# Performance work log

Measured on AMD Instinct MI355X. Metric: run time of the kernel, lower is better.

## Reference

```python
import jax, jax.numpy as jnp
import numpy as np

N_NODES = 100000


def gcn_conv(x, W, b, src, dst, n_nodes):
    """PyG GCNConv: out = D^{-1/2} (A + I) D^{-1/2} X W + b."""
    h = x @ W  # [N, F_out]
    # add self-loops
    loop = jnp.arange(n_nodes, dtype=src.dtype)
    s = jnp.concatenate([src, loop])
    d = jnp.concatenate([dst, loop])
    # symmetric normalization (deg counts incoming edges incl. self-loop)
    deg = jax.ops.segment_sum(jnp.ones_like(d, dtype=h.dtype), d, num_segments=n_nodes)
    dinv = jnp.where(deg > 0, jax.lax.rsqrt(deg), 0.0)
    coef = dinv[s] * dinv[d]  # [E+N]
    msg = h[s] * coef[:, None]  # gather + scale
    out = jax.ops.segment_sum(msg, d, num_segments=n_nodes)  # scatter-add
    return out + b


def setup_inputs() -> dict:
    key = jax.random.key(0)
    k1, k2, k3, k4, k5, k6 = jax.random.split(key, 6)
    in_dim, hidden_dim, out_dim = 128, 64, 64
    n_edges = 1000000
    x = jax.random.normal(k1, (N_NODES, in_dim), dtype=jnp.float32)
    edge_index = jax.random.randint(k2, (2, n_edges), 0, N_NODES, dtype=jnp.int64)
    # glorot-style init for GCN weights
    W1 = jax.random.normal(k3, (in_dim, hidden_dim), dtype=jnp.float32) / np.sqrt(in_dim)
    b1 = jnp.zeros((hidden_dim,), dtype=jnp.float32)
    W2 = jax.random.normal(k4, (hidden_dim, out_dim), dtype=jnp.float32) / np.sqrt(hidden_dim)
    b2 = jnp.zeros((out_dim,), dtype=jnp.float32)
    return {"x": x, "edge_index": edge_index, "W1": W1, "b1": b1, "W2": W2, "b2": b2}


def reference(x, edge_index, W1, b1, W2, b2):
    src, dst = edge_index[0], edge_index[1]
    h = jax.nn.relu(gcn_conv(x, W1, b1, src, dst, N_NODES))
    out = gcn_conv(h, W2, b2, src, dst, N_NODES)
    return out
```

## Files before the change

kernel.cpp:

```cpp
#include <hip/hip_runtime.h>


#define MD 40
#define NFB 8192

typedef __attribute__((ext_vector_type(8))) short bf16x8;
typedef __attribute__((ext_vector_type(4))) float f32x4;
typedef __attribute__((ext_vector_type(2))) float f32x2;
typedef __attribute__((ext_vector_type(4))) int   i32x4;
typedef __attribute__((ext_vector_type(4))) unsigned u32x4;

__device__ inline unsigned short f2bf(float f) {
    unsigned u = __builtin_bit_cast(unsigned, f);
    unsigned r = (u + 0x7FFFu + ((u >> 16) & 1u)) >> 16;
    return (unsigned short)r;
}

__global__ __launch_bounds__(256) void k_zero_i32(int* __restrict__ p, int n) {
    int i = blockIdx.x * blockDim.x + threadIdx.x;
    if (i < n) p[i] = 0;
}

__device__ inline void convW_one(const float* __restrict__ W, short* __restrict__ Wth,
                                 short* __restrict__ Wtl, int K, int k, int f) {
    float v = W[k * 64 + f];
    unsigned b = __builtin_bit_cast(unsigned, v);
    unsigned hb = b & 0xFFFF0000u;
    float d = v - __builtin_bit_cast(float, hb);
    unsigned lb = __builtin_bit_cast(unsigned, d);
    Wth[f * K + k] = (short)(hb >> 16);
    Wtl[f * K + k] = (short)(lb >> 16);
}

__global__ __launch_bounds__(256) void k_fill_convw(const int* __restrict__ src,
                                                    const int* __restrict__ dst, int E,
                                                    int* __restrict__ cnt,
                                                    int* __restrict__ col_ell, int npx,
                                                    const float* __restrict__ W1,
                                                    short* __restrict__ W1th,
                                                    short* __restrict__ W1tl,
                                                    const float* __restrict__ W2,
                                                    short* __restrict__ W2th,
                                                    short* __restrict__ W2tl) {
    if (blockIdx.x >= NFB) {
        const int b2 = blockIdx.x - NFB;
        if (threadIdx.x < 64) {
            if (b2 < 128) convW_one(W1, W1th, W1tl, 128, b2, threadIdx.x);
            else          convW_one(W2, W2th, W2tl, 64, b2 - 128, threadIdx.x);
        }
        return;
    }
    const int myxcd = blockIdx.x & 7;
    const int lo = myxcd * npx;
    const int hi = lo + npx;
    const int vb = blockIdx.x >> 3;
    const int nvb = NFB >> 3;
    const int tid = vb * 256 + threadIdx.x;
    const int nthr = nvb * 256;
    for (int base = tid * 4; base < E; base += nthr * 4) {
        i32x4 d4 = *(const i32x4*)&dst[base];
#pragma unroll
        for (int k = 0; k < 4; ++k) {
            int d = d4[k];
            if (d >= lo && d < hi) {
                int p = atomicAdd(&cnt[d], 1);
                if (p < MD) col_ell[(size_t)d * MD + p] = src[base + k];
            }
        }
    }
}

template <int K>
__global__ __launch_bounds__(256) void k_mm_f32A(const float* __restrict__ X,
                                                 const short* __restrict__ Wth,
                                                 const short* __restrict__ Wtl,
                                                 const int* __restrict__ cnt,
                                                 unsigned short* __restrict__ G, int n) {
    const int lane = threadIdx.x & 63;
    const int w = threadIdx.x >> 6;
    const int r0 = lane & 15;
    const int kq = lane >> 4;
    const int arow = blockIdx.x * 64 + w * 16 + r0;
    const float* xrow = X + (size_t)(arow < n ? arow : n - 1) * K;

    f32x4 acc[4] = {};
#pragma unroll
    for (int kc = 0; kc < K / 32; ++kc) {
        const int ks = kc * 32 + kq * 8;
        float xv[8];
        *(f32x4*)&xv[0] = __builtin_nontemporal_load((const f32x4*)&xrow[ks]);
        *(f32x4*)&xv[4] = __builtin_nontemporal_load((const f32x4*)&xrow[ks + 4]);
        bf16x8 ah, al;
#pragma unroll
        for (int j = 0; j < 8; ++j) {
            unsigned b = __builtin_bit_cast(unsigned, xv[j]);
            unsigned hb = b & 0xFFFF0000u;
            float d = xv[j] - __builtin_bit_cast(float, hb);
            unsigned lb = __builtin_bit_cast(unsigned, d);
            ah[j] = (short)(hb >> 16);
            al[j] = (short)(lb >> 16);
        }
#pragma unroll
        for (int c = 0; c < 4; ++c) {
            bf16x8 bh = *(const bf16x8*)&Wth[(c * 16 + r0) * K + ks];
            bf16x8 bl = *(const bf16x8*)&Wtl[(c * 16 + r0) * K + ks];
            acc[c] = __builtin_amdgcn_mfma_f32_16x16x32_bf16(ah, bh, acc[c], 0, 0, 0);
            acc[c] = __builtin_amdgcn_mfma_f32_16x16x32_bf16(ah, bl, acc[c], 0, 0, 0);
            acc[c] = __builtin_amdgcn_mfma_f32_16x16x32_bf16(al, bh, acc[c], 0, 0, 0);
        }
    }
    const int orow = blockIdx.x * 64 + w * 16 + kq * 4;
#pragma unroll
    for (int rg = 0; rg < 4; ++rg) {
        int gr = orow + rg;
        if (gr < n) {
            float di = rsqrtf((float)(cnt[gr] + 1));
#pragma unroll
            for (int c = 0; c < 4; ++c)
                G[(size_t)gr * 64 + c * 16 + r0] = f2bf(acc[c][rg] * di);
        }
    }
}

__global__ __launch_bounds__(256) void k_mm_bf16A(const unsigned short* __restrict__ A,
                                                  const short* __restrict__ Wth,
                                                  const short* __restrict__ Wtl,
                                                  const int* __restrict__ cnt,
                                                  unsigned short* __restrict__ G, int n) {
    constexpr int K = 64;
    const int lane = threadIdx.x & 63;
    const int w = threadIdx.x >> 6;
    const int r0 = lane & 15;
    const int kq = lane >> 4;
    const int arow = blockIdx.x * 64 + w * 16 + r0;
    const unsigned short* ar = A + (size_t)(arow < n ? arow : n - 1) * K;

    f32x4 acc[4] = {};
#pragma unroll
    for (int kc = 0; kc < K / 32; ++kc) {
        const int ks = kc * 32 + kq * 8;
        bf16x8 a = __builtin_nontemporal_load((const bf16x8*)&ar[ks]);
#pragma unroll
        for (int c = 0; c < 4; ++c) {
            bf16x8 bh = *(const bf16x8*)&Wth[(c * 16 + r0) * K + ks];
            bf16x8 bl = *(const bf16x8*)&Wtl[(c * 16 + r0) * K + ks];
            acc[c] = __builtin_amdgcn_mfma_f32_16x16x32_bf16(a, bh, acc[c], 0, 0, 0);
            acc[c] = __builtin_amdgcn_mfma_f32_16x16x32_bf16(a, bl, acc[c], 0, 0, 0);
        }
    }
    const int orow = blockIdx.x * 64 + w * 16 + kq * 4;
#pragma unroll
    for (int rg = 0; rg < 4; ++rg) {
        int gr = orow + rg;
        if (gr < n) {
            float di = rsqrtf((float)(cnt[gr] + 1));
#pragma unroll
            for (int c = 0; c < 4; ++c)
                G[(size_t)gr * 64 + c * 16 + r0] = f2bf(acc[c][rg] * di);
        }
    }
}

template <bool RELU, bool OUTBF>
__global__ __launch_bounds__(256) void k_gather8(const unsigned short* __restrict__ g,
                                                 const int* __restrict__ cntArr,
                                                 const int* __restrict__ col_ell,
                                                 const float* __restrict__ bias,
                                                 void* __restrict__ dest, int n, int npx) {
    const int b = blockIdx.x;
    const int node = (b & 7) * npx + ((b >> 3) << 2) + (threadIdx.x >> 6);
    if (node >= n) return;
    const int lane = threadIdx.x & 63;
    const int grp = lane >> 3;
    const int fl = lane & 7;
    const int cn = cntArr[node];
    const int lc = min(cn, MD);
    const float dn = rsqrtf((float)(cn + 1));
    const int myidx = col_ell[(size_t)node * MD + lane];

    f32x2 acc2[4] = {};
    if (grp == 0) {
        u32x4 u = *(const u32x4*)&g[(size_t)node * 64 + fl * 8];
#pragma unroll
        for (int k = 0; k < 4; ++k) {
            acc2[k][0] = __builtin_bit_cast(float, u[k] << 16);
            acc2[k][1] = __builtin_bit_cast(float, u[k] & 0xFFFF0000u);
        }
    }
    for (int j8 = 0; j8 < lc; j8 += 8) {
        int j = j8 + grp;
        int s = __shfl(myidx, j);
        if (j < lc) {
            u32x4 u = *(const u32x4*)&g[(size_t)s * 64 + fl * 8];
#pragma unroll
            for (int k = 0; k < 4; ++k) {
                f32x2 f;
                f[0] = __builtin_bit_cast(float, u[k] << 16);
                f[1] = __builtin_bit_cast(float, u[k] & 0xFFFF0000u);
                acc2[k] += f;
            }
        }
    }
#pragma unroll
    for (int m = 8; m <= 32; m <<= 1) {
#pragma unroll
        for (int k = 0; k < 4; ++k) {
            f32x2 o;
            o[0] = __shfl_xor(acc2[k][0], m);
            o[1] = __shfl_xor(acc2[k][1], m);
            acc2[k] += o;
        }
    }
    if (grp == 0) {
        float v[8];
        const float* bv = &bias[fl * 8];
#pragma unroll
        for (int k = 0; k < 4; ++k) {
            v[2 * k]     = fmaf(acc2[k][0], dn, bv[2 * k]);
            v[2 * k + 1] = fmaf(acc2[k][1], dn, bv[2 * k + 1]);
            if (RELU) {
                v[2 * k]     = fmaxf(v[2 * k], 0.f);
                v[2 * k + 1] = fmaxf(v[2 * k + 1], 0.f);
            }
        }
        if (OUTBF) {
            u32x4 o;
            o[0] = (unsigned)f2bf(v[0]) | ((unsigned)f2bf(v[1]) << 16);
            o[1] = (unsigned)f2bf(v[2]) | ((unsigned)f2bf(v[3]) << 16);
            o[2] = (unsigned)f2bf(v[4]) | ((unsigned)f2bf(v[5]) << 16);
            o[3] = (unsigned)f2bf(v[6]) | ((unsigned)f2bf(v[7]) << 16);
            *(u32x4*)&((unsigned short*)dest)[(size_t)node * 64 + fl * 8] = o;
        } else {
            float* dp = &((float*)dest)[(size_t)node * 64 + fl * 8];
            __builtin_nontemporal_store(*(const f32x4*)&v[0], (f32x4*)&dp[0]);
            __builtin_nontemporal_store(*(const f32x4*)&v[4], (f32x4*)&dp[4]);
        }
    }
}

extern "C" void kernel_launch(void* const* d_in, const int* in_sizes, int n_in,
                              void* d_out, int out_size, void* d_ws, size_t ws_size,
                              hipStream_t stream) {
    const float* x  = (const float*)d_in[0];
    const int*   ei = (const int*)d_in[1];
    const float* W1 = (const float*)d_in[2];
    const float* b1 = (const float*)d_in[3];
    const float* W2 = (const float*)d_in[4];
    const float* b2 = (const float*)d_in[5];

    const int N = in_sizes[0] / 128;
    const int E = in_sizes[1] / 2;
    const int* src = ei;
    const int* dst = ei + E;
    float* out = (float*)d_out;

    char* ws = (char*)d_ws;
    size_t off = 0;
    auto alloc = [&](size_t bytes) {
        void* p = ws + off;
        off += (bytes + 63) & ~(size_t)63;
        return p;
    };
    unsigned short* a1   = (unsigned short*)alloc((size_t)N * 64 * 2);
    unsigned short* gbuf = (unsigned short*)alloc((size_t)N * 64 * 2);
    int*   cnt     = (int*)alloc((size_t)N * 4);
    int*   col_ell = (int*)alloc(((size_t)N * MD + 64) * 4);
    short* W1th    = (short*)alloc((size_t)64 * 128 * 2);
    short* W1tl    = (short*)alloc((size_t)64 * 128 * 2);
    short* W2th    = (short*)alloc((size_t)64 * 64 * 2);
    short* W2tl    = (short*)alloc((size_t)64 * 64 * 2);

    const int NBZ   = (N + 255) / 256;
    const int NB_MM = (N + 63) / 64;
    const int npx   = (N + 7) / 8;
    const int NB_G  = 8 * ((npx + 3) / 4);

    k_zero_i32<<<NBZ, 256, 0, stream>>>(cnt, N);

    k_fill_convw<<<NFB + 192, 256, 0, stream>>>(src, dst, E, cnt, col_ell, npx,
                                                W1, W1th, W1tl, W2, W2th, W2tl);

    k_mm_f32A<128><<<NB_MM, 256, 0, stream>>>(x, W1th, W1tl, cnt, gbuf, N);
    k_gather8<true, true><<<NB_G, 256, 0, stream>>>(gbuf, cnt, col_ell, b1, a1, N, npx);

    k_mm_bf16A<<<NB_MM, 256, 0, stream>>>(a1, W2th, W2tl, cnt, gbuf, N);
    k_gather8<false, false><<<NB_G, 256, 0, stream>>>(gbuf, cnt, col_ell, b2, out, N, npx);
}
```

Before: 186.7 us.

## Reorder layer-2 as aggregate-then-transform and fuse the W2 matmul into the gather

Layer 2 now aggregates the normalized bf16 activations first and then multiplies by W2 inside the gather kernel, holding W2 in shared memory. This removes the separate layer-2 matmul kernel, the write and read of its intermediate buffer, and the W2 hi/lo split conversion. The first gather pre-scales its output by dinv so the second gather can sum neighbours directly. In exchange each gather block does 64x64 FMAs per node through shuffles, plus a 16KB shared-memory load of W2 per block, and the matmul now runs in fp32 on CUDA cores instead of MFMA.

```diff
diff --git a/kernel.cpp b/kernel.cpp
--- a/kernel.cpp
+++ b/kernel.cpp
@@ -38,16 +38,10 @@
                                                     int* __restrict__ col_ell, int npx,
                                                     const float* __restrict__ W1,
                                                     short* __restrict__ W1th,
-                                                    short* __restrict__ W1tl,
-                                                    const float* __restrict__ W2,
-                                                    short* __restrict__ W2th,
-                                                    short* __restrict__ W2tl) {
+                                                    short* __restrict__ W1tl) {
     if (blockIdx.x >= NFB) {
         const int b2 = blockIdx.x - NFB;
-        if (threadIdx.x < 64) {
-            if (b2 < 128) convW_one(W1, W1th, W1tl, 128, b2, threadIdx.x);
-            else          convW_one(W2, W2th, W2tl, 64, b2 - 128, threadIdx.x);
-        }
+        if (threadIdx.x < 64) convW_one(W1, W1th, W1tl, 128, b2, threadIdx.x);
         return;
     }
     const int myxcd = blockIdx.x & 7;
@@ -122,51 +116,12 @@
     }
 }
 
-__global__ __launch_bounds__(256) void k_mm_bf16A(const unsigned short* __restrict__ A,
-                                                  const short* __restrict__ Wth,
-                                                  const short* __restrict__ Wtl,
-                                                  const int* __restrict__ cnt,
-                                                  unsigned short* __restrict__ G, int n) {
-    constexpr int K = 64;
-    const int lane = threadIdx.x & 63;
-    const int w = threadIdx.x >> 6;
-    const int r0 = lane & 15;
-    const int kq = lane >> 4;
-    const int arow = blockIdx.x * 64 + w * 16 + r0;
-    const unsigned short* ar = A + (size_t)(arow < n ? arow : n - 1) * K;
-
-    f32x4 acc[4] = {};
-#pragma unroll
-    for (int kc = 0; kc < K / 32; ++kc) {
-        const int ks = kc * 32 + kq * 8;
-        bf16x8 a = __builtin_nontemporal_load((const bf16x8*)&ar[ks]);
-#pragma unroll
-        for (int c = 0; c < 4; ++c) {
-            bf16x8 bh = *(const bf16x8*)&Wth[(c * 16 + r0) * K + ks];
-            bf16x8 bl = *(const bf16x8*)&Wtl[(c * 16 + r0) * K + ks];
-            acc[c] = __builtin_amdgcn_mfma_f32_16x16x32_bf16(a, bh, acc[c], 0, 0, 0);
-            acc[c] = __builtin_amdgcn_mfma_f32_16x16x32_bf16(a, bl, acc[c], 0, 0, 0);
-        }
-    }
-    const int orow = blockIdx.x * 64 + w * 16 + kq * 4;
-#pragma unroll
-    for (int rg = 0; rg < 4; ++rg) {
-        int gr = orow + rg;
-        if (gr < n) {
-            float di = rsqrtf((float)(cnt[gr] + 1));
-#pragma unroll
-            for (int c = 0; c < 4; ++c)
-                G[(size_t)gr * 64 + c * 16 + r0] = f2bf(acc[c][rg] * di);
-        }
-    }
-}
-
-template <bool RELU, bool OUTBF>
-__global__ __launch_bounds__(256) void k_gather8(const unsigned short* __restrict__ g,
+__global__ __launch_bounds__(256) void k_gather1(const unsigned short* __restrict__ g,
                                                  const int* __restrict__ cntArr,
                                                  const int* __restrict__ col_ell,
                                                  const float* __restrict__ bias,
-                                                 void* __restrict__ dest, int n, int npx) {
+                                                 unsigned short* __restrict__ dest,
+                                                 int n, int npx) {
     const int b = blockIdx.x;
     const int node = (b & 7) * npx + ((b >> 3) << 2) + (threadIdx.x >> 6);
     if (node >= n) return;
@@ -212,30 +167,89 @@
         }
     }
     if (grp == 0) {
-        float v[8];
         const float* bv = &bias[fl * 8];
-#pragma unroll
-        for (int k = 0; k < 4; ++k) {
-            v[2 * k]     = fmaf(acc2[k][0], dn, bv[2 * k]);
-            v[2 * k + 1] = fmaf(acc2[k][1], dn, bv[2 * k + 1]);
-            if (RELU) {
-                v[2 * k]     = fmaxf(v[2 * k], 0.f);
-                v[2 * k + 1] = fmaxf(v[2 * k + 1], 0.f);
+        u32x4 o;
+#pragma unroll
+        for (int k = 0; k < 4; ++k) {
+            float v0 = fmaxf(fmaf(acc2[k][0], dn, bv[2 * k]), 0.f) * dn;
+            float v1 = fmaxf(fmaf(acc2[k][1], dn, bv[2 * k + 1]), 0.f) * dn;
+            o[k] = (unsigned)f2bf(v0) | ((unsigned)f2bf(v1) << 16);
+        }
+        *(u32x4*)&dest[(size_t)node * 64 + fl * 8] = o;
+    }
+}
+
+__global__ __launch_bounds__(256) void k_gather_mm(const unsigned short* __restrict__ a,
+                                                   const int* __restrict__ cntArr,
+                                                   const int* __restrict__ col_ell,
+                                                   const float* __restrict__ W2,
+                                                   const float* __restrict__ b2,
+                                                   float* __restrict__ out,
+                                                   int n, int npx) {
+    __shared__ float W2s[64 * 64];
+    {
+        const f32x4* s4 = (const f32x4*)W2;
+        f32x4* d4 = (f32x4*)W2s;
+        for (int i = threadIdx.x; i < 1024; i += 256) d4[i] = s4[i];
+    }
+    __syncthreads();
+
+    const int b = blockIdx.x;
+    const int node = (b & 7) * npx + ((b >> 3) << 2) + (threadIdx.x >> 6);
+    if (node >= n) return;
+    const int lane = threadIdx.x & 63;
+    const int grp = lane >> 3;
+    const int fl = lane & 7;
+    const int cn = cntArr[node];
+    const int lc = min(cn, MD);
+    const float dn = rsqrtf((float)(cn + 1));
+    const int myidx = col_ell[(size_t)node * MD + lane];
+
+    f32x2 acc2[4] = {};
+    if (grp == 0) {
+        u32x4 u = *(const u32x4*)&a[(size_t)node * 64 + fl * 8];
+#pragma unroll
+        for (int k = 0; k < 4; ++k) {
+            acc2[k][0] = __builtin_bit_cast(float, u[k] << 16);
+            acc2[k][1] = __builtin_bit_cast(float, u[k] & 0xFFFF0000u);
+        }
+    }
+    for (int j8 = 0; j8 < lc; j8 += 8) {
+        int j = j8 + grp;
+        int s = __shfl(myidx, j);
+        if (j < lc) {
+            u32x4 u = *(const u32x4*)&a[(size_t)s * 64 + fl * 8];
+#pragma unroll
+            for (int k = 0; k < 4; ++k) {
+                f32x2 f;
+                f[0] = __builtin_bit_cast(float, u[k] << 16);
+                f[1] = __builtin_bit_cast(float, u[k] & 0xFFFF0000u);
+                acc2[k] += f;
             }
         }
-        if (OUTBF) {
-            u32x4 o;
-            o[0] = (unsigned)f2bf(v[0]) | ((unsigned)f2bf(v[1]) << 16);
-            o[1] = (unsigned)f2bf(v[2]) | ((unsigned)f2bf(v[3]) << 16);
-            o[2] = (unsigned)f2bf(v[4]) | ((unsigned)f2bf(v[5]) << 16);
-            o[3] = (unsigned)f2bf(v[6]) | ((unsigned)f2bf(v[7]) << 16);
-            *(u32x4*)&((unsigned short*)dest)[(size_t)node * 64 + fl * 8] = o;
-        } else {
-            float* dp = &((float*)dest)[(size_t)node * 64 + fl * 8];
-            __builtin_nontemporal_store(*(const f32x4*)&v[0], (f32x4*)&dp[0]);
-            __builtin_nontemporal_store(*(const f32x4*)&v[4], (f32x4*)&dp[4]);
-        }
-    }
+    }
+#pragma unroll
+    for (int m = 8; m <= 32; m <<= 1) {
+#pragma unroll
+        for (int k = 0; k < 4; ++k) {
+            f32x2 o;
+            o[0] = __shfl_xor(acc2[k][0], m);
+            o[1] = __shfl_xor(acc2[k][1], m);
+            acc2[k] += o;
+        }
+    }
+    float o = 0.f;
+#pragma unroll
+    for (int j = 0; j < 8; ++j) {
+        const float vj = acc2[j >> 1][j & 1];
+#pragma unroll
+        for (int h = 0; h < 8; ++h) {
+            float bc = __shfl(vj, h);
+            o = fmaf(bc, W2s[(h * 8 + j) * 64 + lane], o);
+        }
+    }
+    float res = fmaf(o, dn, b2[lane]);
+    __builtin_nontemporal_store(res, &out[(size_t)node * 64 + lane]);
 }
 
 extern "C" void kernel_launch(void* const* d_in, const int* in_sizes, int n_in,
@@ -267,8 +281,6 @@
     int*   col_ell = (int*)alloc(((size_t)N * MD + 64) * 4);
     short* W1th    = (short*)alloc((size_t)64 * 128 * 2);
     short* W1tl    = (short*)alloc((size_t)64 * 128 * 2);
-    short* W2th    = (short*)alloc((size_t)64 * 64 * 2);
-    short* W2tl    = (short*)alloc((size_t)64 * 64 * 2);
 
     const int NBZ   = (N + 255) / 256;
     const int NB_MM = (N + 63) / 64;
@@ -277,12 +289,11 @@
 
     k_zero_i32<<<NBZ, 256, 0, stream>>>(cnt, N);
 
-    k_fill_convw<<<NFB + 192, 256, 0, stream>>>(src, dst, E, cnt, col_ell, npx,
-                                                W1, W1th, W1tl, W2, W2th, W2tl);
+    k_fill_convw<<<NFB + 128, 256, 0, stream>>>(src, dst, E, cnt, col_ell, npx,
+                                                W1, W1th, W1tl);
 
     k_mm_f32A<128><<<NB_MM, 256, 0, stream>>>(x, W1th, W1tl, cnt, gbuf, N);
-    k_gather8<true, true><<<NB_G, 256, 0, stream>>>(gbuf, cnt, col_ell, b1, a1, N, npx);
-
-    k_mm_bf16A<<<NB_MM, 256, 0, stream>>>(a1, W2th, W2tl, cnt, gbuf, N);
-    k_gather8<false, false><<<NB_G, 256, 0, stream>>>(gbuf, cnt, col_ell, b2, out, N, npx);
-}
+    k_gather1<<<NB_G, 256, 0, stream>>>(gbuf, cnt, col_ell, b1, a1, N, npx);
+
+    k_gather_mm<<<NB_G, 256, 0, stream>>>(a1, cnt, col_ell, W2, b2, out, N, npx);
+}
```

Measured after the change: 251.1 us. 34.5% more time.
